# Optimization experiments

Measured on AMD Instinct MI355X. Metric: run time of the kernel, lower is better.

Reference implementation:

```python
import jax, jax.numpy as jnp
import numpy as np

N = 100000
E = 1600000
IN_C, HID, OUT_C = 40, 64, 3


def _glorot(key, shape):
    fan_in, fan_out = shape[1], shape[0]
    lim = float(np.sqrt(6.0 / (fan_in + fan_out)))
    return jax.random.uniform(key, shape, jnp.float32, -lim, lim)


def setup_inputs() -> dict:
    key = jax.random.key(0)
    ks = jax.random.split(key, 12)
    x = jax.random.normal(ks[0], (N, IN_C), dtype=jnp.float32)
    edge_index = jax.random.randint(ks[1], (2, E), 0, N, dtype=jnp.int64)
    # Layer dims: 40->64, 64->128, 128->3. PyG SAGEConv: lin_l (neighbor, with bias), lin_r (root, no bias).
    params = {
        'W1l': _glorot(ks[2], (HID, IN_C)), 'b1': jnp.zeros((HID,), jnp.float32), 'W1r': _glorot(ks[3], (HID, IN_C)),
        'W2l': _glorot(ks[4], (2 * HID, HID)), 'b2': jnp.zeros((2 * HID,), jnp.float32), 'W2r': _glorot(ks[5], (2 * HID, HID)),
        'W4l': _glorot(ks[6], (OUT_C, 2 * HID)), 'b4': jnp.zeros((OUT_C,), jnp.float32), 'W4r': _glorot(ks[7], (OUT_C, 2 * HID)),
    }
    return {'x': x, 'edge_index': edge_index, **params}


def _sage_conv(x, src, dst, deg_inv, Wl, bl, Wr):
    # mean-aggregate neighbor messages x[src] at dst, then lin_l(agg) + lin_r(x) + b
    msgs = x[src]                                            # [E, F]
    agg = jax.ops.segment_sum(msgs, dst, num_segments=N)     # [N, F]
    mean = agg * deg_inv[:, None]
    return mean @ Wl.T + bl + x @ Wr.T


def reference(x, edge_index, W1l, b1, W1r, W2l, b2, W2r, W4l, b4, W4r):
    src, dst = edge_index[0], edge_index[1]
    deg = jax.ops.segment_sum(jnp.ones((E,), x.dtype), dst, num_segments=N)
    deg_inv = jnp.where(deg > 0, 1.0 / jnp.maximum(deg, 1.0), 0.0)
    h = jax.nn.relu(_sage_conv(x, src, dst, deg_inv, W1l, b1, W1r))
    h = jax.nn.relu(_sage_conv(h, src, dst, deg_inv, W2l, b2, W2r))
    h = _sage_conv(h, src, dst, deg_inv, W4l, b4, W4r)
    return h
```

## Files before the change

### kernel.cpp

```cpp
#include <hip/hip_runtime.h>
#include <hip/hip_bf16.h>


static constexpr int NN = 100000;
static constexpr int EE = 1600000;
static constexpr int NRANGE = 256;
static constexpr int RSIZE = (NN + NRANGE - 1) / NRANGE;
static constexpr int RPAD = 512;
static constexpr int NBUCKET = 8 * NRANGE;
static constexpr int CAP = 1024;
static constexpr int BCHUNK = 2048;
static constexpr int BUCKET_BLOCKS = (EE + BCHUNK - 1) / BCHUNK;
static constexpr int CVT_BLOCKS = (NN * 40 / 8 + 255) / 256;
static constexpr int NCHUNK = NN / 32;

typedef __attribute__((ext_vector_type(8))) short short8;
typedef __attribute__((ext_vector_type(4))) float f32x4;

__device__ __forceinline__ float bf2f(unsigned short u) {
    union { unsigned int i; float f; } c; c.i = ((unsigned int)u) << 16; return c.f;
}
__device__ __forceinline__ unsigned short f2bf(float f) {
    union { float f; unsigned int i; } c; c.f = f;
    unsigned int x = c.i;
    return (unsigned short)((x + 0x7fffu + ((x >> 16) & 1u)) >> 16);
}

__global__ __launch_bounds__(256) void k_bucket_cvt(const int* __restrict__ src, const int* __restrict__ dst,
                                                    int* __restrict__ pcur, unsigned int* __restrict__ pairs,
                                                    const float* __restrict__ x, unsigned short* __restrict__ xb) {
    __shared__ int cnt[NRANGE];
    __shared__ int base[NRANGE];
    const int tid = threadIdx.x;
    if (blockIdx.x >= BUCKET_BLOCKS) {
        int i = (blockIdx.x - BUCKET_BLOCKS) * 256 + tid;
        if (i < NN * 40 / 8) {
            const float4* p = (const float4*)(x + (size_t)i * 8);
            float4 a = p[0], b = p[1];
            short8 v;
            v[0] = (short)f2bf(a.x); v[1] = (short)f2bf(a.y); v[2] = (short)f2bf(a.z); v[3] = (short)f2bf(a.w);
            v[4] = (short)f2bf(b.x); v[5] = (short)f2bf(b.y); v[6] = (short)f2bf(b.z); v[7] = (short)f2bf(b.w);
            *(short8*)(xb + (size_t)i * 8) = v;
        }
        return;
    }
    const int part = blockIdx.x & 7;
    const int e0 = blockIdx.x * BCHUNK;
    cnt[tid] = 0;
    __syncthreads();
    int r_[8], lp_[8];
    unsigned int p_[8];
#pragma unroll
    for (int j = 0; j < 8; ++j) {
        int e = e0 + j * 256 + tid;
        r_[j] = -1;
        if (e < EE) {
            int d = dst[e];
            int s = src[e];
            int r = d / RSIZE;
            r_[j] = r;
            p_[j] = (unsigned int)s | ((unsigned int)(d - r * RSIZE) << 17);
            lp_[j] = atomicAdd(&cnt[r], 1);
        }
    }
    __syncthreads();
    {
        int c = cnt[tid];
        base[tid] = (c > 0) ? atomicAdd(&pcur[(part << 8) | tid], c) : 0;
    }
    __syncthreads();
#pragma unroll
    for (int j = 0; j < 8; ++j) {
        if (r_[j] >= 0) {
            int pos = base[r_[j]] + lp_[j];
            if (pos < CAP) pairs[(size_t)((part << 8) | r_[j]) * CAP + pos] = p_[j];
        }
    }
}

__global__ __launch_bounds__(1024) void k_build(const unsigned int* __restrict__ pairs,
                                                const int* __restrict__ pcur,
                                                int* __restrict__ row_start, float* __restrict__ deg_inv,
                                                int* __restrict__ csr_src) {
    __shared__ int ldeg[RPAD];
    __shared__ int lrs[RPAD];
    __shared__ int rtot[NRANGE];
    const int tid = threadIdx.x;
    const int r = blockIdx.x;
    const int lo = r * RSIZE;
    const int nloc = (lo + RSIZE <= NN) ? RSIZE : (NN - lo);
    for (int t = tid; t < RPAD; t += 1024) ldeg[t] = 0;
    __syncthreads();
    for (int p = 0; p < 8; ++p) {
        int b = (p << 8) | r;
        int len = pcur[b]; if (len > CAP) len = CAP;
        const unsigned int* bp = pairs + (size_t)b * CAP;
        for (int i = tid; i < len; i += 1024)
            atomicAdd(&ldeg[bp[i] >> 17], 1);
    }
    if (tid < NRANGE) {
        int s = 0;
#pragma unroll
        for (int p = 0; p < 8; ++p) {
            int c = pcur[(p << 8) | tid];
            s += (c > CAP) ? CAP : c;
        }
        rtot[tid] = s;
    }
    __syncthreads();
    for (int d = 1; d < NRANGE; d <<= 1) {
        int t = (tid < NRANGE && tid >= d) ? rtot[tid - d] : 0;
        __syncthreads();
        if (tid < NRANGE) rtot[tid] += t;
        __syncthreads();
    }
    const int rbase = (r == 0) ? 0 : rtot[r - 1];
    if (tid < RPAD) lrs[tid] = ldeg[tid];
    __syncthreads();
    for (int d = 1; d < RPAD; d <<= 1) {
        int t = (tid < RPAD && tid >= d) ? lrs[tid - d] : 0;
        __syncthreads();
        if (tid < RPAD) lrs[tid] += t;
        __syncthreads();
    }
    int excl = 0, dg = 0;
    if (tid < RPAD) { dg = ldeg[tid]; excl = lrs[tid] - dg; }
    if (tid < nloc) {
        row_start[lo + tid] = rbase + excl;
        deg_inv[lo + tid] = (dg > 0) ? 1.0f / (float)dg : 0.0f;
    }
    if (r == 0 && tid == 0) row_start[NN] = EE;
    __syncthreads();
    if (tid < RPAD) { lrs[tid] = excl; ldeg[tid] = 0; }
    __syncthreads();
    for (int p = 0; p < 8; ++p) {
        int b = (p << 8) | r;
        int len = pcur[b]; if (len > CAP) len = CAP;
        const unsigned int* bp = pairs + (size_t)b * CAP;
        for (int i = tid; i < len; i += 1024) {
            unsigned int pk = bp[i];
            int dloc = pk >> 17;
            int lp = atomicAdd(&ldeg[dloc], 1);
            csr_src[rbase + lrs[dloc] + lp] = (int)(pk & 0x1FFFFu);
        }
    }
}

template<int Fin, int Fout, bool RELU, bool ZR>
__global__ __launch_bounds__(256) void k_fused(const unsigned short* __restrict__ xin,
                                               const int* __restrict__ row_start,
                                               const int* __restrict__ csr_src,
                                               const float* __restrict__ deg_inv,
                                               const float* __restrict__ Wl,
                                               const float* __restrict__ bias,
                                               const float* __restrict__ Wr,
                                               unsigned short* __restrict__ out,
                                               const float* __restrict__ W4l,
                                               const float* __restrict__ W4r,
                                               float* __restrict__ z,
                                               float* __restrict__ rr_) {
    constexpr int KS = 4;
    constexpr int TILES = Fout / 16;
    constexpr int TPW = TILES / 4;
    constexpr int WB = TILES * KS * 64 * 8;
    constexpr int SMEAN = 0;
    constexpr int SROOT = 32 * 72;
    constexpr int SH2 = 2 * 32 * 72;
    constexpr int STEADY = 2 * 32 * 72 + (ZR ? 32 * 136 : 0);
    constexpr int FILL = WB + (ZR ? 4 * 64 * 8 : 0);
    constexpr int SHM = (STEADY > FILL) ? STEADY : FILL;
    __shared__ short shm[SHM];
    const int tid = threadIdx.x;
    const int lane = tid & 63;
    const int wv = tid >> 6;

    for (int idx = tid; idx < TILES * KS * 64; idx += 256) {
        int l = idx & 63;
        int ks = (idx >> 6) % KS;
        int t = idx / (64 * KS);
        int o = t * 16 + (l & 15);
        int kbase = ks * 32 + (l >> 4) * 8;
        short8 v;
#pragma unroll
        for (int j = 0; j < 8; ++j) {
            int k = kbase + j;
            float w;
            if (k < 64) w = (k < Fin) ? Wl[(size_t)o * Fin + k] : 0.f;
            else { int k2 = k - 64; w = (k2 < Fin) ? Wr[(size_t)o * Fin + k2] : 0.f; }
            v[j] = (short)f2bf(w);
        }
        *(short8*)&shm[idx * 8] = v;
    }
    if constexpr (ZR) {
        for (int idx = tid; idx < 4 * 64; idx += 256) {
            int l = idx & 63;
            int ks = idx >> 6;
            int o = l & 15;
            int kbase = ks * 32 + (l >> 4) * 8;
            short8 v;
#pragma unroll
            for (int j = 0; j < 8; ++j) {
                int k = kbase + j;
                float w = 0.f;
                if (o < 3) w = W4l[o * 128 + k];
                else if (o >= 4 && o < 7) w = W4r[(o - 4) * 128 + k];
                v[j] = (short)f2bf(w);
            }
            *(short8*)&shm[WB + idx * 8] = v;
        }
    }
    __syncthreads();
    short8 bfr[TPW][KS];
#pragma unroll
    for (int tt = 0; tt < TPW; ++tt)
#pragma unroll
        for (int ks = 0; ks < KS; ++ks)
            bfr[tt][ks] = *(const short8*)&shm[(((wv * TPW + tt) * KS + ks) * 64 + lane) * 8];
    short8 b4r[4];
    if constexpr (ZR) {
        if (wv < 2) {
#pragma unroll
            for (int ks = 0; ks < 4; ++ks)
                b4r[ks] = *(const short8*)&shm[WB + (ks * 64 + lane) * 8];
        }
    }
    float bias_t[TPW];
#pragma unroll
    for (int tt = 0; tt < TPW; ++tt) bias_t[tt] = bias[(wv * TPW + tt) * 16 + (lane & 15)];
    __syncthreads();

    const int node8 = tid >> 3;
    const int c = tid & 7;

    for (int ci = blockIdx.x; ci < NCHUNK; ci += gridDim.x) {
        const int nbase = ci * 32;
        {
            const int node = nbase + node8;
            float acc[8] = {0, 0, 0, 0, 0, 0, 0, 0};
            short8 rv = {0, 0, 0, 0, 0, 0, 0, 0};
            if (c * 8 < Fin) {
                const unsigned short* xq = xin + c * 8;
                int rs = row_start[node], re = row_start[node + 1];
                int k = rs;
                for (; k + 4 <= re; k += 4) {
                    int s0 = csr_src[k], s1 = csr_src[k + 1], s2 = csr_src[k + 2], s3 = csr_src[k + 3];
                    short8 v0 = *(const short8*)(xq + (size_t)s0 * Fin);
                    short8 v1 = *(const short8*)(xq + (size_t)s1 * Fin);
                    short8 v2 = *(const short8*)(xq + (size_t)s2 * Fin);
                    short8 v3 = *(const short8*)(xq + (size_t)s3 * Fin);
#pragma unroll
                    for (int j = 0; j < 8; ++j)
                        acc[j] += (bf2f((unsigned short)v0[j]) + bf2f((unsigned short)v1[j]))
                                + (bf2f((unsigned short)v2[j]) + bf2f((unsigned short)v3[j]));
                }
                for (; k < re; ++k) {
                    short8 v0 = *(const short8*)(xq + (size_t)csr_src[k] * Fin);
#pragma unroll
                    for (int j = 0; j < 8; ++j) acc[j] += bf2f((unsigned short)v0[j]);
                }
                float di = deg_inv[node];
#pragma unroll
                for (int j = 0; j < 8; ++j) acc[j] *= di;
                rv = *(const short8*)(xin + (size_t)node * Fin + c * 8);
            }
            short8 mv;
#pragma unroll
            for (int j = 0; j < 8; ++j) mv[j] = (c * 8 < Fin) ? (short)f2bf(acc[j]) : (short)0;
            *(short8*)&shm[SMEAN + node8 * 72 + c * 8] = mv;
            *(short8*)&shm[SROOT + node8 * 72 + c * 8] = rv;
        }
        __syncthreads();
        short8 af[2][KS];
#pragma unroll
        for (int ks = 0; ks < KS; ++ks) {
            const int base = (ks < 2) ? SMEAN : SROOT;
            const int g = (ks & 1) * 4 + (lane >> 4);
            af[0][ks] = *(const short8*)&shm[base + (lane & 15) * 72 + g * 8];
            af[1][ks] = *(const short8*)&shm[base + (16 + (lane & 15)) * 72 + g * 8];
        }
        f32x4 acc2[2][TPW];
#pragma unroll
        for (int m = 0; m < 2; ++m)
#pragma unroll
            for (int tt = 0; tt < TPW; ++tt) acc2[m][tt] = (f32x4){0.f, 0.f, 0.f, 0.f};
#pragma unroll
        for (int tt = 0; tt < TPW; ++tt)
#pragma unroll
            for (int ks = 0; ks < KS; ++ks) {
                acc2[0][tt] = __builtin_amdgcn_mfma_f32_16x16x32_bf16(af[0][ks], bfr[tt][ks], acc2[0][tt], 0, 0, 0);
                acc2[1][tt] = __builtin_amdgcn_mfma_f32_16x16x32_bf16(af[1][ks], bfr[tt][ks], acc2[1][tt], 0, 0, 0);
            }
        if constexpr (!ZR) {
#pragma unroll
            for (int m = 0; m < 2; ++m) {
                int nrow = nbase + m * 16 + (lane >> 4) * 4;
#pragma unroll
                for (int tt = 0; tt < TPW; ++tt) {
                    int col = (wv * TPW + tt) * 16 + (lane & 15);
#pragma unroll
                    for (int q = 0; q < 4; ++q) {
                        float v = acc2[m][tt][q] + bias_t[tt];
                        if (RELU) v = fmaxf(v, 0.f);
                        out[(size_t)(nrow + q) * Fout + col] = f2bf(v);
                    }
                }
            }
        } else {
#pragma unroll
            for (int m = 0; m < 2; ++m) {
                int row0 = m * 16 + (lane >> 4) * 4;
#pragma unroll
                for (int tt = 0; tt < TPW; ++tt) {
                    int col = (wv * TPW + tt) * 16 + (lane & 15);
#pragma unroll
                    for (int q = 0; q < 4; ++q) {
                        float v = acc2[m][tt][q] + bias_t[tt];
                        if (RELU) v = fmaxf(v, 0.f);
                        shm[SH2 + (row0 + q) * 136 + col] = (short)f2bf(v);
                    }
                }
            }
            __syncthreads();
            if (wv < 2) {
                const int row = wv * 16 + (lane & 15);
                f32x4 az = (f32x4){0.f, 0.f, 0.f, 0.f};
#pragma unroll
                for (int ks = 0; ks < 4; ++ks) {
                    short8 a4 = *(const short8*)&shm[SH2 + row * 136 + (ks * 4 + (lane >> 4)) * 8];
                    az = __builtin_amdgcn_mfma_f32_16x16x32_bf16(a4, b4r[ks], az, 0, 0, 0);
                }
                const int col = lane & 15;
                const int nr = nbase + wv * 16 + (lane >> 4) * 4;
                if (col < 3) {
#pragma unroll
                    for (int q = 0; q < 4; ++q) z[(size_t)(nr + q) * 4 + col] = az[q];
                } else if (col >= 4 && col < 7) {
#pragma unroll
                    for (int q = 0; q < 4; ++q) rr_[(size_t)(nr + q) * 4 + col - 4] = az[q];
                }
            }
        }
        __syncthreads();
    }
}

__global__ __launch_bounds__(256) void k_final(const float* __restrict__ z, const float* __restrict__ r,
                                               const float* __restrict__ b4,
                                               const int* __restrict__ row_start, const int* __restrict__ csr_src,
                                               const float* __restrict__ deg_inv, float* __restrict__ out) {
    int n = blockIdx.x * 256 + threadIdx.x;
    if (n >= NN) return;
    int rs = row_start[n], re = row_start[n + 1];
    float a0 = 0, a1 = 0, a2 = 0, b0 = 0, b1 = 0, b2 = 0;
    int k = rs;
    for (; k + 4 <= re; k += 4) {
        int s0 = csr_src[k], s1 = csr_src[k + 1], s2 = csr_src[k + 2], s3 = csr_src[k + 3];
        float4 z0 = *(const float4*)&z[4 * (size_t)s0];
        float4 z1 = *(const float4*)&z[4 * (size_t)s1];
        float4 z2 = *(const float4*)&z[4 * (size_t)s2];
        float4 z3 = *(const float4*)&z[4 * (size_t)s3];
        a0 += z0.x; a1 += z0.y; a2 += z0.z;
        b0 += z1.x; b1 += z1.y; b2 += z1.z;
        a0 += z2.x; a1 += z2.y; a2 += z2.z;
        b0 += z3.x; b1 += z3.y; b2 += z3.z;
    }
    for (; k < re; ++k) {
        float4 z0 = *(const float4*)&z[4 * (size_t)csr_src[k]];
        a0 += z0.x; a1 += z0.y; a2 += z0.z;
    }
    float di = deg_inv[n];
    float4 rn = *(const float4*)&r[4 * (size_t)n];
    out[(size_t)n * 3 + 0] = (a0 + b0) * di + rn.x + b4[0];
    out[(size_t)n * 3 + 1] = (a1 + b1) * di + rn.y + b4[1];
    out[(size_t)n * 3 + 2] = (a2 + b2) * di + rn.z + b4[2];
}

extern "C" void kernel_launch(void* const* d_in, const int* in_sizes, int n_in,
                              void* d_out, int out_size, void* d_ws, size_t ws_size,
                              hipStream_t stream) {
    const float* x   = (const float*)d_in[0];
    const int*   ei  = (const int*)d_in[1];
    const float* W1l = (const float*)d_in[2];
    const float* b1  = (const float*)d_in[3];
    const float* W1r = (const float*)d_in[4];
    const float* W2l = (const float*)d_in[5];
    const float* b2  = (const float*)d_in[6];
    const float* W2r = (const float*)d_in[7];
    const float* W4l = (const float*)d_in[8];
    const float* b4  = (const float*)d_in[9];
    const float* W4r = (const float*)d_in[10];
    float* out = (float*)d_out;

    char* ws = (char*)d_ws;
    size_t off = 0;
    auto alloc = [&](size_t bytes) -> void* {
        void* p = ws + off;
        off = (off + bytes + 255) & ~(size_t)255;
        return p;
    };
    int*   row_start = (int*)alloc(((size_t)NN + 1) * 4);
    int*   csr_src   = (int*)alloc((size_t)EE * 4);
    float* deg_inv   = (float*)alloc((size_t)NN * 4);
    int*   pcur      = (int*)alloc((size_t)NBUCKET * 4);
    unsigned short* xb = (unsigned short*)alloc((size_t)NN * 40 * 2);
    unsigned short* h1 = (unsigned short*)alloc((size_t)NN * 64 * 2);
    float* zbuf = (float*)alloc((size_t)NN * 4 * 4);
    float* rbuf = (float*)alloc((size_t)NN * 4 * 4);
    unsigned int* pairs = (unsigned int*)alloc((size_t)NBUCKET * CAP * 4);

    const int* e_src = ei;
    const int* e_dst = ei + EE;

    hipMemsetAsync(pcur, 0, (size_t)NBUCKET * 4, stream);

    k_bucket_cvt<<<BUCKET_BLOCKS + CVT_BLOCKS, 256, 0, stream>>>(e_src, e_dst, pcur, pairs, x, xb);
    k_build<<<NRANGE, 1024, 0, stream>>>(pairs, pcur, row_start, deg_inv, csr_src);

    k_fused<40, 64, true, false><<<782, 256, 0, stream>>>(xb, row_start, csr_src, deg_inv,
                                                          W1l, b1, W1r, h1,
                                                          nullptr, nullptr, nullptr, nullptr);
    k_fused<64, 128, true, true><<<782, 256, 0, stream>>>(h1, row_start, csr_src, deg_inv,
                                                          W2l, b2, W2r, nullptr,
                                                          W4l, W4r, zbuf, rbuf);
    k_final<<<(NN + 255) / 256, 256, 0, stream>>>(zbuf, rbuf, b4, row_start, csr_src, deg_inv, out);
}
```

Baseline: 226.6 us.

## Prepack bf16 MFMA weight fragments once and launch one block per chunk

Moves the fp32-to-bf16 weight conversion and MFMA fragment packing out of every fused-layer block into extra blocks of the first bucketing kernel, writing a shared packed buffer that the fused kernels read directly from global memory. This removes per-block weight staging through LDS and the associated barriers, and shrinks LDS use, which may raise occupancy. The fused kernels now launch one block per 32-node chunk instead of a persistent 782-block grid. The MFMA loop is also reordered to load A fragments per k-step, reducing register pressure. Trade-off: more blocks each pay the fragment load cost, though from cache.

```diff
diff --git a/kernel.cpp b/kernel.cpp
--- a/kernel.cpp
+++ b/kernel.cpp
@@ -14,6 +14,13 @@
 static constexpr int CVT_BLOCKS = (NN * 40 / 8 + 255) / 256;
 static constexpr int NCHUNK = NN / 32;
 
+static constexpr int W1OFF = 0;
+static constexpr int W2OFF = 4 * 4 * 64 * 8;
+static constexpr int W4OFF = W2OFF + 8 * 4 * 64 * 8;
+static constexpr int WPACK_SHORTS = W4OFF + 4 * 64 * 8;
+static constexpr int PACK_ITEMS = 4 * 4 * 64 + 8 * 4 * 64 + 4 * 64;
+static constexpr int PACK_BLOCKS = (PACK_ITEMS + 255) / 256;
+
 typedef __attribute__((ext_vector_type(8))) short short8;
 typedef __attribute__((ext_vector_type(4))) float f32x4;
 
@@ -28,10 +35,60 @@
 
 __global__ __launch_bounds__(256) void k_bucket_cvt(const int* __restrict__ src, const int* __restrict__ dst,
                                                     int* __restrict__ pcur, unsigned int* __restrict__ pairs,
-                                                    const float* __restrict__ x, unsigned short* __restrict__ xb) {
+                                                    const float* __restrict__ x, unsigned short* __restrict__ xb,
+                                                    const float* __restrict__ W1l, const float* __restrict__ W1r,
+                                                    const float* __restrict__ W2l, const float* __restrict__ W2r,
+                                                    const float* __restrict__ W4l, const float* __restrict__ W4r,
+                                                    unsigned short* __restrict__ wpack) {
     __shared__ int cnt[NRANGE];
     __shared__ int base[NRANGE];
     const int tid = threadIdx.x;
+    if (blockIdx.x >= BUCKET_BLOCKS + CVT_BLOCKS) {
+        int idx = (blockIdx.x - BUCKET_BLOCKS - CVT_BLOCKS) * 256 + tid;
+        if (idx < PACK_ITEMS) {
+            short8 v;
+            if (idx < 1024) {
+                int l = idx & 63, ks = (idx >> 6) & 3, t = idx >> 8;
+                int o = t * 16 + (l & 15);
+                int kbase = ks * 32 + (l >> 4) * 8;
+#pragma unroll
+                for (int j = 0; j < 8; ++j) {
+                    int k = kbase + j; float w;
+                    if (k < 64) w = (k < 40) ? W1l[o * 40 + k] : 0.f;
+                    else { int k2 = k - 64; w = (k2 < 40) ? W1r[o * 40 + k2] : 0.f; }
+                    v[j] = (short)f2bf(w);
+                }
+                *(short8*)&wpack[W1OFF + idx * 8] = v;
+            } else if (idx < 3072) {
+                int i2 = idx - 1024;
+                int l = i2 & 63, ks = (i2 >> 6) & 3, t = i2 >> 8;
+                int o = t * 16 + (l & 15);
+                int kbase = ks * 32 + (l >> 4) * 8;
+#pragma unroll
+                for (int j = 0; j < 8; ++j) {
+                    int k = kbase + j;
+                    float w = (k < 64) ? W2l[o * 64 + k] : W2r[o * 64 + (k - 64)];
+                    v[j] = (short)f2bf(w);
+                }
+                *(short8*)&wpack[W2OFF + i2 * 8] = v;
+            } else {
+                int i4 = idx - 3072;
+                int l = i4 & 63, ks = i4 >> 6;
+                int o = l & 15;
+                int kbase = ks * 32 + (l >> 4) * 8;
+#pragma unroll
+                for (int j = 0; j < 8; ++j) {
+                    int k = kbase + j;
+                    float w = 0.f;
+                    if (o < 3) w = W4l[o * 128 + k];
+                    else if (o >= 4 && o < 7) w = W4r[(o - 4) * 128 + k];
+                    v[j] = (short)f2bf(w);
+                }
+                *(short8*)&wpack[W4OFF + i4 * 8] = v;
+            }
+        }
+        return;
+    }
     if (blockIdx.x >= BUCKET_BLOCKS) {
         int i = (blockIdx.x - BUCKET_BLOCKS) * 256 + tid;
         if (i < NN * 40 / 8) {
@@ -146,88 +203,45 @@
     }
 }
 
-template<int Fin, int Fout, bool RELU, bool ZR>
+template<int Fin, int Fout, bool RELU, bool ZR, int WOFF>
 __global__ __launch_bounds__(256) void k_fused(const unsigned short* __restrict__ xin,
                                                const int* __restrict__ row_start,
                                                const int* __restrict__ csr_src,
                                                const float* __restrict__ deg_inv,
-                                               const float* __restrict__ Wl,
+                                               const unsigned short* __restrict__ wpack,
                                                const float* __restrict__ bias,
-                                               const float* __restrict__ Wr,
                                                unsigned short* __restrict__ out,
-                                               const float* __restrict__ W4l,
-                                               const float* __restrict__ W4r,
                                                float* __restrict__ z,
                                                float* __restrict__ rr_) {
     constexpr int KS = 4;
     constexpr int TILES = Fout / 16;
     constexpr int TPW = TILES / 4;
-    constexpr int WB = TILES * KS * 64 * 8;
     constexpr int SMEAN = 0;
     constexpr int SROOT = 32 * 72;
     constexpr int SH2 = 2 * 32 * 72;
-    constexpr int STEADY = 2 * 32 * 72 + (ZR ? 32 * 136 : 0);
-    constexpr int FILL = WB + (ZR ? 4 * 64 * 8 : 0);
-    constexpr int SHM = (STEADY > FILL) ? STEADY : FILL;
+    constexpr int SHM = 2 * 32 * 72 + (ZR ? 32 * 136 : 0);
     __shared__ short shm[SHM];
     const int tid = threadIdx.x;
     const int lane = tid & 63;
     const int wv = tid >> 6;
 
-    for (int idx = tid; idx < TILES * KS * 64; idx += 256) {
-        int l = idx & 63;
-        int ks = (idx >> 6) % KS;
-        int t = idx / (64 * KS);
-        int o = t * 16 + (l & 15);
-        int kbase = ks * 32 + (l >> 4) * 8;
-        short8 v;
-#pragma unroll
-        for (int j = 0; j < 8; ++j) {
-            int k = kbase + j;
-            float w;
-            if (k < 64) w = (k < Fin) ? Wl[(size_t)o * Fin + k] : 0.f;
-            else { int k2 = k - 64; w = (k2 < Fin) ? Wr[(size_t)o * Fin + k2] : 0.f; }
-            v[j] = (short)f2bf(w);
-        }
-        *(short8*)&shm[idx * 8] = v;
-    }
-    if constexpr (ZR) {
-        for (int idx = tid; idx < 4 * 64; idx += 256) {
-            int l = idx & 63;
-            int ks = idx >> 6;
-            int o = l & 15;
-            int kbase = ks * 32 + (l >> 4) * 8;
-            short8 v;
-#pragma unroll
-            for (int j = 0; j < 8; ++j) {
-                int k = kbase + j;
-                float w = 0.f;
-                if (o < 3) w = W4l[o * 128 + k];
-                else if (o >= 4 && o < 7) w = W4r[(o - 4) * 128 + k];
-                v[j] = (short)f2bf(w);
-            }
-            *(short8*)&shm[WB + idx * 8] = v;
-        }
-    }
-    __syncthreads();
     short8 bfr[TPW][KS];
 #pragma unroll
     for (int tt = 0; tt < TPW; ++tt)
 #pragma unroll
         for (int ks = 0; ks < KS; ++ks)
-            bfr[tt][ks] = *(const short8*)&shm[(((wv * TPW + tt) * KS + ks) * 64 + lane) * 8];
+            bfr[tt][ks] = *(const short8*)&wpack[WOFF + (((wv * TPW + tt) * KS + ks) * 64 + lane) * 8];
     short8 b4r[4];
     if constexpr (ZR) {
         if (wv < 2) {
 #pragma unroll
             for (int ks = 0; ks < 4; ++ks)
-                b4r[ks] = *(const short8*)&shm[WB + (ks * 64 + lane) * 8];
+                b4r[ks] = *(const short8*)&wpack[W4OFF + (ks * 64 + lane) * 8];
         }
     }
     float bias_t[TPW];
 #pragma unroll
     for (int tt = 0; tt < TPW; ++tt) bias_t[tt] = bias[(wv * TPW + tt) * 16 + (lane & 15)];
-    __syncthreads();
 
     const int node8 = tid >> 3;
     const int c = tid & 7;
@@ -270,26 +284,23 @@
             *(short8*)&shm[SROOT + node8 * 72 + c * 8] = rv;
         }
         __syncthreads();
-        short8 af[2][KS];
+        f32x4 acc2[2][TPW];
+#pragma unroll
+        for (int m = 0; m < 2; ++m)
+#pragma unroll
+            for (int tt = 0; tt < TPW; ++tt) acc2[m][tt] = (f32x4){0.f, 0.f, 0.f, 0.f};
 #pragma unroll
         for (int ks = 0; ks < KS; ++ks) {
             const int base = (ks < 2) ? SMEAN : SROOT;
             const int g = (ks & 1) * 4 + (lane >> 4);
-            af[0][ks] = *(const short8*)&shm[base + (lane & 15) * 72 + g * 8];
-            af[1][ks] = *(const short8*)&shm[base + (16 + (lane & 15)) * 72 + g * 8];
-        }
-        f32x4 acc2[2][TPW];
-#pragma unroll
-        for (int m = 0; m < 2; ++m)
-#pragma unroll
-            for (int tt = 0; tt < TPW; ++tt) acc2[m][tt] = (f32x4){0.f, 0.f, 0.f, 0.f};
-#pragma unroll
-        for (int tt = 0; tt < TPW; ++tt)
-#pragma unroll
-            for (int ks = 0; ks < KS; ++ks) {
-                acc2[0][tt] = __builtin_amdgcn_mfma_f32_16x16x32_bf16(af[0][ks], bfr[tt][ks], acc2[0][tt], 0, 0, 0);
-                acc2[1][tt] = __builtin_amdgcn_mfma_f32_16x16x32_bf16(af[1][ks], bfr[tt][ks], acc2[1][tt], 0, 0, 0);
-            }
+            short8 a0 = *(const short8*)&shm[base + (lane & 15) * 72 + g * 8];
+            short8 a1 = *(const short8*)&shm[base + (16 + (lane & 15)) * 72 + g * 8];
+#pragma unroll
+            for (int tt = 0; tt < TPW; ++tt) {
+                acc2[0][tt] = __builtin_amdgcn_mfma_f32_16x16x32_bf16(a0, bfr[tt][ks], acc2[0][tt], 0, 0, 0);
+                acc2[1][tt] = __builtin_amdgcn_mfma_f32_16x16x32_bf16(a1, bfr[tt][ks], acc2[1][tt], 0, 0, 0);
+            }
+        }
         if constexpr (!ZR) {
 #pragma unroll
             for (int m = 0; m < 2; ++m) {
@@ -402,8 +413,9 @@
     int*   csr_src   = (int*)alloc((size_t)EE * 4);
     float* deg_inv   = (float*)alloc((size_t)NN * 4);
     int*   pcur      = (int*)alloc((size_t)NBUCKET * 4);
-    unsigned short* xb = (unsigned short*)alloc((size_t)NN * 40 * 2);
-    unsigned short* h1 = (unsigned short*)alloc((size_t)NN * 64 * 2);
+    unsigned short* xb    = (unsigned short*)alloc((size_t)NN * 40 * 2);
+    unsigned short* h1    = (unsigned short*)alloc((size_t)NN * 64 * 2);
+    unsigned short* wpack = (unsigned short*)alloc((size_t)WPACK_SHORTS * 2);
     float* zbuf = (float*)alloc((size_t)NN * 4 * 4);
     float* rbuf = (float*)alloc((size_t)NN * 4 * 4);
     unsigned int* pairs = (unsigned int*)alloc((size_t)NBUCKET * CAP * 4);
@@ -413,14 +425,13 @@
 
     hipMemsetAsync(pcur, 0, (size_t)NBUCKET * 4, stream);
 
-    k_bucket_cvt<<<BUCKET_BLOCKS + CVT_BLOCKS, 256, 0, stream>>>(e_src, e_dst, pcur, pairs, x, xb);
+    k_bucket_cvt<<<BUCKET_BLOCKS + CVT_BLOCKS + PACK_BLOCKS, 256, 0, stream>>>(
+        e_src, e_dst, pcur, pairs, x, xb, W1l, W1r, W2l, W2r, W4l, W4r, wpack);
     k_build<<<NRANGE, 1024, 0, stream>>>(pairs, pcur, row_start, deg_inv, csr_src);
 
-    k_fused<40, 64, true, false><<<782, 256, 0, stream>>>(xb, row_start, csr_src, deg_inv,
-                                                          W1l, b1, W1r, h1,
-                                                          nullptr, nullptr, nullptr, nullptr);
-    k_fused<64, 128, true, true><<<782, 256, 0, stream>>>(h1, row_start, csr_src, deg_inv,
-                                                          W2l, b2, W2r, nullptr,
-                                                          W4l, W4r, zbuf, rbuf);
+    k_fused<40, 64, true, false, W1OFF><<<NCHUNK, 256, 0, stream>>>(
+        xb, row_start, csr_src, deg_inv, wpack, b1, h1, nullptr, nullptr);
+    k_fused<64, 128, true, true, W2OFF><<<NCHUNK, 256, 0, stream>>>(
+        h1, row_start, csr_src, deg_inv, wpack, b2, nullptr, zbuf, rbuf);
     k_final<<<(NN + 255) / 256, 256, 0, stream>>>(zbuf, rbuf, b4, row_start, csr_src, deg_inv, out);
 }
```

After: 208.9 us. 7.8% less time.
